# Kernel tuning notes

Hardware: AMD Instinct MI355X
Metric: run time of the kernel (lower is better)

## Reference

```python
import jax, jax.numpy as jnp
import numpy as np
from jax.scipy.special import logsumexp

# Circuit configuration (matches init_kwargs)
V, K, C = 256, 32, 256        # num_vars, input nodes per var, num categories
N = V * K                     # nodes per layer (8192)
E, PF, SF, L = 32768, 4, 16, 5  # elements/layer, prod fan-in, sum fan-in, layer pairs
B = 512                       # batch size


def setup_inputs() -> dict:
    key = jax.random.key(0)
    k0, k1, k2, k3, k4, k5 = jax.random.split(key, 6)
    inputs = jax.random.randint(k0, (B, V), 0, C)                     # [B, num_vars]
    input_logps = jax.nn.log_softmax(jax.random.normal(k1, (V, K, C)), axis=-1)
    prod_children = jax.random.randint(k2, (L, E, PF), 0, N)          # element -> child nodes
    sum_children = jax.random.randint(k3, (L, N, SF), 0, E)           # sum node -> child elements
    sum_logw = jax.nn.log_softmax(jax.random.normal(k4, (L, N, SF)), axis=-1)
    root_logw = jax.nn.log_softmax(jax.random.normal(k5, (N,)))
    return {"inputs": inputs, "input_logps": input_logps,
            "prod_children": prod_children, "sum_children": sum_children,
            "sum_logw": sum_logw, "root_logw": root_logw}


def reference(inputs, input_logps, prod_children, sum_children, sum_logw, root_logw):
    V_, K_, C_ = input_logps.shape
    B_ = inputs.shape[0]
    N_ = V_ * K_

    # ---- input layer: node_mars[v*K+k, b] = log p_{v,k}(inputs[b, v]) ----
    idx = jnp.broadcast_to(inputs.T[:, None, :], (V_, K_, B_))        # [V, K, B]
    node_mars = jnp.take_along_axis(input_logps, idx, axis=2)         # [V, K, B]
    node_mars = node_mars.reshape(N_, B_)                             # [num_nodes, B]

    # ---- inner layers: alternating product (segment log-sum) / sum (logsumexp) ----
    def layer(nm, xs):
        pc, sc, lw = xs                                               # [E,PF], [N,SF], [N,SF]
        element_mars = nm[pc].sum(axis=1)                             # prod: [E, PF, B] -> [E, B]
        nm_next = logsumexp(element_mars[sc] + lw[..., None], axis=1) # sum:  [N, SF, B] -> [N, B]
        return nm_next, None

    node_mars, _ = jax.lax.scan(layer, node_mars, (prod_children, sum_children, sum_logw))
    # ---- root sum node over all last-layer nodes ----
    lls = logsumexp(node_mars + root_logw[:, None], axis=0)           # [B]
    return lls[:, None]                                               # [B, num_roots=1]
```

## Files before the change

### kernel.cpp

```cpp
#include <hip/hip_runtime.h>
#include <hip/hip_fp16.h>

namespace {

constexpr int V_ = 256, K_ = 32, C_ = 256;
constexpr int N_ = V_ * K_;
constexpr int E_ = 32768, PF_ = 4, SF_ = 16, L_ = 5;
constexpr int B_ = 512;
constexpr int NSLICE = B_ / 8;
constexpr int NCHK = 4;
constexpr int NPB = N_ / NCHK;

constexpr int PREP_T  = L_ * N_ * SF_;
constexpr int INPUT_T = NSLICE * N_;

constexpr float LOG2E = 1.4426950408889634f;
constexpr float LN2   = 0.6931471805599453f;

typedef _Float16 h2v __attribute__((ext_vector_type(2)));

__device__ __forceinline__ uint32_t f2h(float a, float b) {
    __half2 h = __floats2half2_rn(a, b);
    return *reinterpret_cast<uint32_t*>(&h);
}
__device__ __forceinline__ h2v splat2h(uint32_t bits) {
    const _Float16 h = __builtin_bit_cast(_Float16, (unsigned short)(bits & 0xffffu));
    h2v r; r.x = h; r.y = h; return r;
}
__device__ __forceinline__ float2 h2f2(h2v v) {
    return make_float2((float)v.x, (float)v.y);
}
__device__ __forceinline__ h2v u2h(uint32_t u) { return __builtin_bit_cast(h2v, u); }

__global__ void setup_k(const int* __restrict__ sc,
                        const int* __restrict__ pc,
                        const float* __restrict__ lw,
                        const float* __restrict__ rw,
                        const int* __restrict__ inp,
                        const float* __restrict__ lp,
                        ushort4* __restrict__ pcx,
                        __half* __restrict__ lwh,
                        uint4* __restrict__ nm)
{
    const int t = blockIdx.x * blockDim.x + threadIdx.x;
    if (t < PREP_T) {
        const int l = t >> 17;
        const int n = (t >> 4) & (N_ - 1);
        const int e = sc[t];
        const int4 p = *reinterpret_cast<const int4*>(pc + ((size_t)l * E_ + e) * 4);
        ushort4 u;
        u.x = (unsigned short)p.x; u.y = (unsigned short)p.y;
        u.z = (unsigned short)p.z; u.w = (unsigned short)p.w;
        pcx[t] = u;
        const float add = (l == L_ - 1) ? rw[n] : 0.f;
        lwh[t] = __float2half((lw[t] + add) * LOG2E);
    } else {
        const int t2 = t - PREP_T;
        const int vk = t2 & (N_ - 1);
        const int bs = t2 >> 13;
        const int v = vk >> 5;
        const int b = bs * 8;
        const float* row = lp + (size_t)vk * C_;
        uint4 r;
        r.x = f2h(row[inp[(b + 0) * V_ + v]] * LOG2E, row[inp[(b + 1) * V_ + v]] * LOG2E);
        r.y = f2h(row[inp[(b + 2) * V_ + v]] * LOG2E, row[inp[(b + 3) * V_ + v]] * LOG2E);
        r.z = f2h(row[inp[(b + 4) * V_ + v]] * LOG2E, row[inp[(b + 5) * V_ + v]] * LOG2E);
        r.w = f2h(row[inp[(b + 6) * V_ + v]] * LOG2E, row[inp[(b + 7) * V_ + v]] * LOG2E);
        nm[(size_t)bs * N_ + vk] = r;
    }
}

__device__ __forceinline__ void node_lse(const uint4* lds, const uint4* pr, const uint4* wr,
                                         h2v m2[4], float acc[8])
{
    h2v xs[8][4], cm[4];

    auto children8 = [&](const uint4 pw0, const uint4 pw1, const uint4 pw2,
                         const uint4 pw3, const uint4 wv) {
        auto child = [&](int s8, uint32_t rr0, uint32_t rr1, uint32_t wbits) {
            const uint4 a = lds[rr0 & 0xffffu];
            const uint4 b = lds[rr0 >> 16];
            const uint4 c = lds[rr1 & 0xffffu];
            const uint4 d = lds[rr1 >> 16];
            const h2v w2 = splat2h(wbits);
            #pragma unroll
            for (int q = 0; q < 4; ++q) {
                h2v t = (u2h((&a.x)[q]) + u2h((&b.x)[q]))
                      + (u2h((&c.x)[q]) + u2h((&d.x)[q]));
                t = t + w2;
                xs[s8][q] = t;
                cm[q] = __builtin_elementwise_max(cm[q], t);
            }
        };
        child(0, pw0.x, pw0.y, wv.x);
        child(1, pw0.z, pw0.w, wv.x >> 16);
        child(2, pw1.x, pw1.y, wv.y);
        child(3, pw1.z, pw1.w, wv.y >> 16);
        child(4, pw2.x, pw2.y, wv.z);
        child(5, pw2.z, pw2.w, wv.z >> 16);
        child(6, pw3.x, pw3.y, wv.w);
        child(7, pw3.z, pw3.w, wv.w >> 16);
    };

    #pragma unroll
    for (int q = 0; q < 4; ++q) cm[q] = splat2h(0xF400u);
    children8(pr[0], pr[1], pr[2], pr[3], wr[0]);
    #pragma unroll
    for (int q = 0; q < 4; ++q) m2[q] = cm[q];
    #pragma unroll
    for (int j = 0; j < 8; ++j) acc[j] = 0.f;
    #pragma unroll
    for (int s = 0; s < 8; ++s) {
        #pragma unroll
        for (int q = 0; q < 4; ++q) {
            const float2 f = h2f2(xs[s][q] - m2[q]);
            acc[2 * q + 0] += exp2f(f.x);
            acc[2 * q + 1] += exp2f(f.y);
        }
    }

    #pragma unroll
    for (int q = 0; q < 4; ++q) cm[q] = splat2h(0xF400u);
    children8(pr[4], pr[5], pr[6], pr[7], wr[1]);
    #pragma unroll
    for (int q = 0; q < 4; ++q) {
        const h2v mm = __builtin_elementwise_max(m2[q], cm[q]);
        const float2 df = h2f2(m2[q] - mm);
        acc[2 * q + 0] *= exp2f(df.x);
        acc[2 * q + 1] *= exp2f(df.y);
        m2[q] = mm;
    }
    #pragma unroll
    for (int s = 0; s < 8; ++s) {
        #pragma unroll
        for (int q = 0; q < 4; ++q) {
            const float2 f = h2f2(xs[s][q] - m2[q]);
            acc[2 * q + 0] += exp2f(f.x);
            acc[2 * q + 1] += exp2f(f.y);
        }
    }
}

__global__ __launch_bounds__(1024) void layer_k(
    const uint4* __restrict__ nmi,
    const uint4* __restrict__ pcx,
    const uint4* __restrict__ lwh,
    uint4* __restrict__ nmo)
{
    __shared__ uint4 lds[N_];
    const int bs = blockIdx.x & (NSLICE - 1);
    const int nc = blockIdx.x >> 6;

    const uint4* src = nmi + (size_t)bs * N_;
    for (int i = threadIdx.x; i < N_; i += 1024) lds[i] = src[i];
    __syncthreads();

    #pragma unroll
    for (int r = 0; r < 2; ++r) {
        const int n = nc * NPB + r * 1024 + threadIdx.x;
        h2v m2[4];
        float acc[8];
        node_lse(lds, pcx + (size_t)n * 8, lwh + (size_t)n * 2, m2, acc);

        uint4 o;
        {
            const float2 f0 = h2f2(m2[0]);
            const float2 f1 = h2f2(m2[1]);
            o.x = f2h(f0.x + log2f(acc[0]), f0.y + log2f(acc[1]));
            o.y = f2h(f1.x + log2f(acc[2]), f1.y + log2f(acc[3]));
        }
        {
            const float2 f2v = h2f2(m2[2]);
            const float2 f3v = h2f2(m2[3]);
            o.z = f2h(f2v.x + log2f(acc[4]), f2v.y + log2f(acc[5]));
            o.w = f2h(f3v.x + log2f(acc[6]), f3v.y + log2f(acc[7]));
        }
        nmo[(size_t)bs * N_ + n] = o;
    }
}

__global__ __launch_bounds__(1024) void layer_last_k(
    const uint4* __restrict__ nmi,
    const uint4* __restrict__ pcx,
    const uint4* __restrict__ lwh,
    float* __restrict__ pm,
    float* __restrict__ ps)
{
    __shared__ uint4 lds[N_];
    const int bs = blockIdx.x & (NSLICE - 1);
    const int nc = blockIdx.x >> 6;

    const uint4* src = nmi + (size_t)bs * N_;
    for (int i = threadIdx.x; i < N_; i += 1024) lds[i] = src[i];
    __syncthreads();

    float v0[8];
    {
        const int n = nc * NPB + threadIdx.x;
        h2v m2[4];
        float acc[8];
        node_lse(lds, pcx + (size_t)n * 8, lwh + (size_t)n * 2, m2, acc);
        #pragma unroll
        for (int q = 0; q < 4; ++q) {
            const float2 f = h2f2(m2[q]);
            v0[2 * q + 0] = f.x + log2f(acc[2 * q + 0]);
            v0[2 * q + 1] = f.y + log2f(acc[2 * q + 1]);
        }
    }
    float M[8], S[8];
    {
        const int n = nc * NPB + 1024 + threadIdx.x;
        h2v m2[4];
        float acc[8];
        node_lse(lds, pcx + (size_t)n * 8, lwh + (size_t)n * 2, m2, acc);
        #pragma unroll
        for (int q = 0; q < 4; ++q) {
            const float2 f = h2f2(m2[q]);
            const float v1a = f.x + log2f(acc[2 * q + 0]);
            const float v1b = f.y + log2f(acc[2 * q + 1]);
            M[2 * q + 0] = fmaxf(v0[2 * q + 0], v1a);
            M[2 * q + 1] = fmaxf(v0[2 * q + 1], v1b);
            S[2 * q + 0] = exp2f(v0[2 * q + 0] - M[2 * q + 0]) + exp2f(v1a - M[2 * q + 0]);
            S[2 * q + 1] = exp2f(v0[2 * q + 1] - M[2 * q + 1]) + exp2f(v1b - M[2 * q + 1]);
        }
    }

    for (int d = 1; d < 64; d <<= 1) {
        #pragma unroll
        for (int j = 0; j < 8; ++j) {
            const float om = __shfl_xor(M[j], d);
            const float os = __shfl_xor(S[j], d);
            const float nmax = fmaxf(M[j], om);
            S[j] = S[j] * exp2f(M[j] - nmax) + os * exp2f(om - nmax);
            M[j] = nmax;
        }
    }

    __syncthreads();
    float* red = reinterpret_cast<float*>(lds);
    const int wid = threadIdx.x >> 6;
    if ((threadIdx.x & 63) == 0) {
        #pragma unroll
        for (int j = 0; j < 8; ++j) {
            red[(wid * 8 + j) * 2 + 0] = M[j];
            red[(wid * 8 + j) * 2 + 1] = S[j];
        }
    }
    __syncthreads();
    if (threadIdx.x < 8) {
        const int j = threadIdx.x;
        float Mm = -3.0e38f, Ss = 0.f;
        for (int w = 0; w < 16; ++w) {
            const float m_ = red[(w * 8 + j) * 2 + 0];
            const float s_ = red[(w * 8 + j) * 2 + 1];
            const float nmax = fmaxf(Mm, m_);
            Ss = Ss * exp2f(Mm - nmax) + s_ * exp2f(m_ - nmax);
            Mm = nmax;
        }
        pm[nc * B_ + bs * 8 + j] = Mm;
        ps[nc * B_ + bs * 8 + j] = Ss;
    }
}

__global__ void root_comb_k(const float* __restrict__ pm,
                            const float* __restrict__ ps,
                            float* __restrict__ out)
{
    const int b = blockIdx.x * blockDim.x + threadIdx.x;
    float M = -3.0e38f, S = 0.f;
    for (int c = 0; c < NCHK; ++c) {
        const float m_ = pm[c * B_ + b];
        const float s_ = ps[c * B_ + b];
        const float nmax = fmaxf(M, m_);
        S = S * exp2f(M - nmax) + s_ * exp2f(m_ - nmax);
        M = nmax;
    }
    out[b] = (M + log2f(S)) * LN2;
}

}

extern "C" void kernel_launch(void* const* d_in, const int* in_sizes, int n_in,
                              void* d_out, int out_size, void* d_ws, size_t ws_size,
                              hipStream_t stream) {
    const int*   inp = (const int*)d_in[0];
    const float* lp  = (const float*)d_in[1];
    const int*   pc  = (const int*)d_in[2];
    const int*   sc  = (const int*)d_in[3];
    const float* lw  = (const float*)d_in[4];
    const float* rw  = (const float*)d_in[5];
    float*       out = (float*)d_out;

    uint4*   nm0 = (uint4*)d_ws;
    uint4*   nm1 = nm0 + (size_t)NSLICE * N_;
    ushort4* pcx = (ushort4*)(nm1 + (size_t)NSLICE * N_);
    __half*  lwh = (__half*)(pcx + (size_t)L_ * N_ * SF_);
    float*   pm  = (float*)(lwh + (size_t)L_ * N_ * SF_);
    float*   ps  = pm + (size_t)NCHK * B_;

    setup_k<<<(PREP_T + INPUT_T) / 256, 256, 0, stream>>>(
        sc, pc, lw, rw, inp, lp, pcx, lwh, nm0);

    for (int l = 0; l < L_ - 1; ++l) {
        const uint4* srcb = (l & 1) ? nm1 : nm0;
        uint4*       dstb = (l & 1) ? nm0 : nm1;
        layer_k<<<NSLICE * NCHK, 1024, 0, stream>>>(
            srcb,
            (const uint4*)(pcx + (size_t)l * N_ * SF_),
            (const uint4*)(lwh + (size_t)l * N_ * SF_),
            dstb);
    }
    layer_last_k<<<NSLICE * NCHK, 1024, 0, stream>>>(
        nm0,
        (const uint4*)(pcx + (size_t)(L_ - 1) * N_ * SF_),
        (const uint4*)(lwh + (size_t)(L_ - 1) * N_ * SF_),
        pm, ps);

    root_comb_k<<<B_ / 256, 256, 0, stream>>>(pm, ps, out);
}
```

Measured before the change: 143.0 us.

## Fuse layer kernels into cooperative persistent kernel with per-slice flag sync

Replaces the five per-layer launches and the root combine launch with a single cooperative kernel. Blocks that share a batch slice synchronise between layers through per-slice atomic counters instead of kernel boundaries, and the root combine is folded into the chunk-0 blocks. This is meant to remove launch gaps and tail effects between layers, in exchange for spin-waiting and a dependence on all 256 blocks being co-resident. The previous multi-kernel path is kept as a fallback if the cooperative launch fails.

```diff
diff --git a/kernel.cpp b/kernel.cpp
--- a/kernel.cpp
+++ b/kernel.cpp
@@ -10,6 +10,7 @@
 constexpr int NSLICE = B_ / 8;
 constexpr int NCHK = 4;
 constexpr int NPB = N_ / NCHK;
+constexpr int NFLAG = NSLICE * L_;
 
 constexpr int PREP_T  = L_ * N_ * SF_;
 constexpr int INPUT_T = NSLICE * N_;
@@ -40,9 +41,11 @@
                         const float* __restrict__ lp,
                         ushort4* __restrict__ pcx,
                         __half* __restrict__ lwh,
-                        uint4* __restrict__ nm)
+                        uint4* __restrict__ nm,
+                        int* __restrict__ flags)
 {
     const int t = blockIdx.x * blockDim.x + threadIdx.x;
+    if (t < NFLAG) flags[t] = 0;
     if (t < PREP_T) {
         const int l = t >> 17;
         const int n = (t >> 4) & (N_ - 1);
@@ -141,16 +144,181 @@
     }
 }
 
-__global__ __launch_bounds__(1024) void layer_k(
-    const uint4* __restrict__ nmi,
+__device__ __forceinline__ void stage_slice(uint4* lds, const uint4* src) {
+    for (int i = threadIdx.x; i < N_; i += 1024) lds[i] = src[i];
+    __syncthreads();
+}
+
+__device__ __forceinline__ void sig_release(int* f) {
+    __threadfence();
+    __syncthreads();
+    if (threadIdx.x == 0) __hip_atomic_fetch_add(f, 1, __ATOMIC_RELEASE,
+                                                 __HIP_MEMORY_SCOPE_AGENT);
+}
+__device__ __forceinline__ void sig_wait(int* f) {
+    if (threadIdx.x == 0) {
+        while (__hip_atomic_load(f, __ATOMIC_ACQUIRE, __HIP_MEMORY_SCOPE_AGENT) < NCHK)
+            __builtin_amdgcn_s_sleep(1);
+    }
+    __syncthreads();
+    __threadfence();
+}
+
+}
+
+__global__ __launch_bounds__(1024) void mega_k(
+    uint4* __restrict__ nm0,
+    uint4* __restrict__ nm1,
     const uint4* __restrict__ pcx,
     const uint4* __restrict__ lwh,
-    uint4* __restrict__ nmo)
+    float* __restrict__ pm,
+    float* __restrict__ ps,
+    float* __restrict__ out,
+    int* __restrict__ flags)
 {
     __shared__ uint4 lds[N_];
     const int bs = blockIdx.x & (NSLICE - 1);
     const int nc = blockIdx.x >> 6;
-
+    int* fl = flags + bs * L_;
+
+    for (int l = 0; l < L_ - 1; ++l) {
+        const uint4* src = ((l & 1) ? nm1 : nm0) + (size_t)bs * N_;
+        uint4*       dst = ((l & 1) ? nm0 : nm1) + (size_t)bs * N_;
+        const uint4* pcl = pcx + (size_t)l * N_ * 8;
+        const uint4* lwl = lwh + (size_t)l * N_ * 2;
+
+        stage_slice(lds, src);
+
+        #pragma unroll
+        for (int r = 0; r < 2; ++r) {
+            const int n = nc * NPB + r * 1024 + threadIdx.x;
+            h2v m2[4];
+            float acc[8];
+            node_lse(lds, pcl + (size_t)n * 8, lwl + (size_t)n * 2, m2, acc);
+
+            uint4 o;
+            {
+                const float2 f0 = h2f2(m2[0]);
+                const float2 f1 = h2f2(m2[1]);
+                o.x = f2h(f0.x + log2f(acc[0]), f0.y + log2f(acc[1]));
+                o.y = f2h(f1.x + log2f(acc[2]), f1.y + log2f(acc[3]));
+            }
+            {
+                const float2 f2v = h2f2(m2[2]);
+                const float2 f3v = h2f2(m2[3]);
+                o.z = f2h(f2v.x + log2f(acc[4]), f2v.y + log2f(acc[5]));
+                o.w = f2h(f3v.x + log2f(acc[6]), f3v.y + log2f(acc[7]));
+            }
+            dst[n] = o;
+        }
+
+        sig_release(fl + l);
+        sig_wait(fl + l);
+    }
+
+    {
+        const int l = L_ - 1;
+        const uint4* src = nm0 + (size_t)bs * N_;
+        const uint4* pcl = pcx + (size_t)l * N_ * 8;
+        const uint4* lwl = lwh + (size_t)l * N_ * 2;
+
+        stage_slice(lds, src);
+
+        float v0[8];
+        {
+            const int n = nc * NPB + threadIdx.x;
+            h2v m2[4];
+            float acc[8];
+            node_lse(lds, pcl + (size_t)n * 8, lwl + (size_t)n * 2, m2, acc);
+            #pragma unroll
+            for (int q = 0; q < 4; ++q) {
+                const float2 f = h2f2(m2[q]);
+                v0[2 * q + 0] = f.x + log2f(acc[2 * q + 0]);
+                v0[2 * q + 1] = f.y + log2f(acc[2 * q + 1]);
+            }
+        }
+        float M[8], S[8];
+        {
+            const int n = nc * NPB + 1024 + threadIdx.x;
+            h2v m2[4];
+            float acc[8];
+            node_lse(lds, pcl + (size_t)n * 8, lwl + (size_t)n * 2, m2, acc);
+            #pragma unroll
+            for (int q = 0; q < 4; ++q) {
+                const float2 f = h2f2(m2[q]);
+                const float v1a = f.x + log2f(acc[2 * q + 0]);
+                const float v1b = f.y + log2f(acc[2 * q + 1]);
+                M[2 * q + 0] = fmaxf(v0[2 * q + 0], v1a);
+                M[2 * q + 1] = fmaxf(v0[2 * q + 1], v1b);
+                S[2 * q + 0] = exp2f(v0[2 * q + 0] - M[2 * q + 0]) + exp2f(v1a - M[2 * q + 0]);
+                S[2 * q + 1] = exp2f(v0[2 * q + 1] - M[2 * q + 1]) + exp2f(v1b - M[2 * q + 1]);
+            }
+        }
+
+        for (int d = 1; d < 64; d <<= 1) {
+            #pragma unroll
+            for (int j = 0; j < 8; ++j) {
+                const float om = __shfl_xor(M[j], d);
+                const float os = __shfl_xor(S[j], d);
+                const float nmax = fmaxf(M[j], om);
+                S[j] = S[j] * exp2f(M[j] - nmax) + os * exp2f(om - nmax);
+                M[j] = nmax;
+            }
+        }
+
+        __syncthreads();
+        float* red = reinterpret_cast<float*>(lds);
+        const int wid = threadIdx.x >> 6;
+        if ((threadIdx.x & 63) == 0) {
+            #pragma unroll
+            for (int j = 0; j < 8; ++j) {
+                red[(wid * 8 + j) * 2 + 0] = M[j];
+                red[(wid * 8 + j) * 2 + 1] = S[j];
+            }
+        }
+        __syncthreads();
+        if (threadIdx.x < 8) {
+            const int j = threadIdx.x;
+            float Mm = -3.0e38f, Ss = 0.f;
+            for (int w = 0; w < 16; ++w) {
+                const float m_ = red[(w * 8 + j) * 2 + 0];
+                const float s_ = red[(w * 8 + j) * 2 + 1];
+                const float nmax = fmaxf(Mm, m_);
+                Ss = Ss * exp2f(Mm - nmax) + s_ * exp2f(m_ - nmax);
+                Mm = nmax;
+            }
+            pm[nc * B_ + bs * 8 + j] = Mm;
+            ps[nc * B_ + bs * 8 + j] = Ss;
+        }
+
+        sig_release(fl + l);
+        if (nc == 0) {
+            sig_wait(fl + l);
+            if (threadIdx.x < 8) {
+                const int b = bs * 8 + threadIdx.x;
+                float Mm = -3.0e38f, Ss = 0.f;
+                for (int c = 0; c < NCHK; ++c) {
+                    const float m_ = pm[c * B_ + b];
+                    const float s_ = ps[c * B_ + b];
+                    const float nmax = fmaxf(Mm, m_);
+                    Ss = Ss * exp2f(Mm - nmax) + s_ * exp2f(m_ - nmax);
+                    Mm = nmax;
+                }
+                out[b] = (Mm + log2f(Ss)) * LN2;
+            }
+        }
+    }
+}
+
+namespace {
+
+__global__ __launch_bounds__(1024) void layer_k(
+    const uint4* __restrict__ nmi, const uint4* __restrict__ pcx,
+    const uint4* __restrict__ lwh, uint4* __restrict__ nmo)
+{
+    __shared__ uint4 lds[N_];
+    const int bs = blockIdx.x & (NSLICE - 1);
+    const int nc = blockIdx.x >> 6;
     const uint4* src = nmi + (size_t)bs * N_;
     for (int i = threadIdx.x; i < N_; i += 1024) lds[i] = src[i];
     __syncthreads();
@@ -161,7 +329,6 @@
         h2v m2[4];
         float acc[8];
         node_lse(lds, pcx + (size_t)n * 8, lwh + (size_t)n * 2, m2, acc);
-
         uint4 o;
         {
             const float2 f0 = h2f2(m2[0]);
@@ -180,16 +347,12 @@
 }
 
 __global__ __launch_bounds__(1024) void layer_last_k(
-    const uint4* __restrict__ nmi,
-    const uint4* __restrict__ pcx,
-    const uint4* __restrict__ lwh,
-    float* __restrict__ pm,
-    float* __restrict__ ps)
+    const uint4* __restrict__ nmi, const uint4* __restrict__ pcx,
+    const uint4* __restrict__ lwh, float* __restrict__ pm, float* __restrict__ ps)
 {
     __shared__ uint4 lds[N_];
     const int bs = blockIdx.x & (NSLICE - 1);
     const int nc = blockIdx.x >> 6;
-
     const uint4* src = nmi + (size_t)bs * N_;
     for (int i = threadIdx.x; i < N_; i += 1024) lds[i] = src[i];
     __syncthreads();
@@ -224,7 +387,6 @@
             S[2 * q + 1] = exp2f(v0[2 * q + 1] - M[2 * q + 1]) + exp2f(v1b - M[2 * q + 1]);
         }
     }
-
     for (int d = 1; d < 64; d <<= 1) {
         #pragma unroll
         for (int j = 0; j < 8; ++j) {
@@ -235,7 +397,6 @@
             M[j] = nmax;
         }
     }
-
     __syncthreads();
     float* red = reinterpret_cast<float*>(lds);
     const int wid = threadIdx.x >> 6;
@@ -262,8 +423,7 @@
     }
 }
 
-__global__ void root_comb_k(const float* __restrict__ pm,
-                            const float* __restrict__ ps,
+__global__ void root_comb_k(const float* __restrict__ pm, const float* __restrict__ ps,
                             float* __restrict__ out)
 {
     const int b = blockIdx.x * blockDim.x + threadIdx.x;
@@ -297,9 +457,23 @@
     __half*  lwh = (__half*)(pcx + (size_t)L_ * N_ * SF_);
     float*   pm  = (float*)(lwh + (size_t)L_ * N_ * SF_);
     float*   ps  = pm + (size_t)NCHK * B_;
+    int*     flags = (int*)(ps + (size_t)NCHK * B_);
 
     setup_k<<<(PREP_T + INPUT_T) / 256, 256, 0, stream>>>(
-        sc, pc, lw, rw, inp, lp, pcx, lwh, nm0);
+        sc, pc, lw, rw, inp, lp, pcx, lwh, nm0, flags);
+
+    int nCU = 0, maxPerCU = 0;
+    bool coop_ok = false;
+    if (hipDeviceGetAttribute(&nCU, hipDeviceAttributeMultiprocessorCount, 0) == hipSuccess &&
+        hipOccupancyMaxActiveBlocksPerMultiprocessor(&maxPerCU, (const void*)mega_k,
+                                                     1024, 0) == hipSuccess &&
+        maxPerCU >= 1 && nCU * maxPerCU >= NSLICE * NCHK) {
+        void* args[] = {(void*)&nm0, (void*)&nm1, (void*)&pcx, (void*)&lwh,
+                        (void*)&pm, (void*)&ps, (void*)&out, (void*)&flags};
+        coop_ok = (hipLaunchCooperativeKernel((const void*)mega_k, dim3(NSLICE * NCHK),
+                                              dim3(1024), args, 0, stream) == hipSuccess);
+    }
+    if (coop_ok) return;
 
     for (int l = 0; l < L_ - 1; ++l) {
         const uint4* srcb = (l & 1) ? nm1 : nm0;
@@ -315,6 +489,5 @@
         (const uint4*)(pcx + (size_t)(L_ - 1) * N_ * SF_),
         (const uint4*)(lwh + (size_t)(L_ - 1) * N_ * SF_),
         pm, ps);
-
     root_comb_k<<<B_ / 256, 256, 0, stream>>>(pm, ps, out);
 }
```

Result: no change. 143.0 us (-0.0%).
